# Kernel tuning notes

Hardware: AMD Instinct MI355X
Metric: run time of the kernel (lower is better)

The kernel has to match this reference:

```python
import jax, jax.numpy as jnp
import numpy as np

INPUT_DIM = 1024
OUTPUT_DIM = 1024
DEGREE = 8


def setup_inputs() -> dict:
    key = jax.random.key(0)
    k1, k2 = jax.random.split(key)
    x = jax.random.normal(k1, (8192, INPUT_DIM), dtype=jnp.float32)
    std = 1.0 / (INPUT_DIM * (DEGREE + 1))
    cheby_coeffs = jax.random.normal(k2, (INPUT_DIM, OUTPUT_DIM, DEGREE + 1), dtype=jnp.float32) * std
    return {"x": x, "cheby_coeffs": cheby_coeffs}


def reference(x, cheby_coeffs):
    # x: [B, I]; cheby_coeffs: [I, O, D+1]
    degree = cheby_coeffs.shape[-1] - 1
    t = jnp.clip(jnp.tanh(x), -0.999, 0.999)            # [B, I]
    theta = jnp.arccos(t)[..., None]                     # [B, I, 1]
    arange = jnp.arange(degree + 1, dtype=x.dtype)       # [D+1]
    basis = jnp.cos(theta * arange)                      # [B, I, D+1] Chebyshev T_d(t)
    y = jnp.einsum('bid,iod->bo', basis, cheby_coeffs)   # [B, O]
    return y
```

## Files before the change

kernel.cpp:

```cpp
#include <hip/hip_runtime.h>
#include <stdint.h>

#define B_ROWS 8192
#define I_DIM  1024
#define N_DIM  1024
#define NDEG   9
#define K_DIM  (I_DIM * (NDEG-1))

typedef __attribute__((ext_vector_type(8)))  short short8;
typedef __attribute__((ext_vector_type(16))) float f32x16;

__device__ __forceinline__ unsigned short f2bf(float f) {
  union { float f; uint32_t u; } v; v.f = f;
  uint32_t u = v.u;
  u += 0x7FFFu + ((u >> 16) & 1u);
  return (unsigned short)(u >> 16);
}

__device__ __forceinline__ float bf2f(unsigned short h) {
  union { uint32_t u; float f; } v; v.u = ((uint32_t)h) << 16;
  return v.f;
}

__device__ __forceinline__ int rowhash(int r) {
  return (r & 7) ^ ((r >> 2) & 4);
}

__global__ __launch_bounds__(256) void basis_kernel(const float* __restrict__ x,
                                                    unsigned short* __restrict__ A) {
  const int b  = blockIdx.x;
  const int i0 = threadIdx.x * 4;
  const float4 xv = *reinterpret_cast<const float4*>(x + (size_t)b * I_DIM + i0);
  float t[4];
  t[0] = fminf(fmaxf(tanhf(xv.x), -0.999f), 0.999f);
  t[1] = fminf(fmaxf(tanhf(xv.y), -0.999f), 0.999f);
  t[2] = fminf(fmaxf(tanhf(xv.z), -0.999f), 0.999f);
  t[3] = fminf(fmaxf(tanhf(xv.w), -0.999f), 0.999f);

  unsigned short* outb = A + (size_t)b * K_DIM + i0;
  float Tp[4] = {1.f, 1.f, 1.f, 1.f};
  float Tc[4] = {t[0], t[1], t[2], t[3]};
  #pragma unroll
  for (int d = 1; d < NDEG; ++d) {
    ushort4 o4;
    o4.x = f2bf(Tc[0]); o4.y = f2bf(Tc[1]); o4.z = f2bf(Tc[2]); o4.w = f2bf(Tc[3]);
    *reinterpret_cast<ushort4*>(outb + (size_t)(d - 1) * I_DIM) = o4;
    if (d < NDEG - 1) {
      #pragma unroll
      for (int j = 0; j < 4; ++j) {
        float Tn = 2.0f * t[j] * Tc[j] - Tp[j];
        Tp[j] = Tc[j]; Tc[j] = Tn;
      }
    }
  }
}

__global__ __launch_bounds__(256) void repack_kernel(const float* __restrict__ cf,
                                                     unsigned short* __restrict__ Bt,
                                                     float* __restrict__ bias) {
  __shared__ unsigned short L[32][584];
  const int i0  = blockIdx.x * 32;
  const int o0  = blockIdx.y * 64;
  const int tid = threadIdx.x;

  #pragma unroll
  for (int j = 0; j < 18; ++j) {
    const int f4  = j * 256 + tid;
    const int il  = f4 / 144;
    const int odq = f4 % 144;
    const float4 v = *reinterpret_cast<const float4*>(
        cf + ((size_t)(i0 + il) * N_DIM + o0) * NDEG + (size_t)odq * 4);
    ushort4 w;
    w.x = f2bf(v.x); w.y = f2bf(v.y); w.z = f2bf(v.z); w.w = f2bf(v.w);
    *reinterpret_cast<ushort4*>(&L[il][odq * 4]) = w;
  }
  __syncthreads();

  for (int od = tid; od < 576; od += 256) {
    const int o = od / 9, d = od % 9;
    if (d == 0) {
      float s = 0.f;
      #pragma unroll
      for (int il = 0; il < 32; ++il) s += bf2f(L[il][od]);
      atomicAdd(&bias[o0 + o], s);
    } else {
      const size_t base = (size_t)(o0 + o) * K_DIM + (size_t)(d - 1) * I_DIM + i0;
      #pragma unroll
      for (int ci = 0; ci < 4; ++ci) {
        uint32_t uu[4];
        #pragma unroll
        for (int p = 0; p < 4; ++p) {
          unsigned short lo = L[ci * 8 + p * 2 + 0][od];
          unsigned short hi = L[ci * 8 + p * 2 + 1][od];
          uu[p] = (uint32_t)lo | ((uint32_t)hi << 16);
        }
        uint4 u; u.x = uu[0]; u.y = uu[1]; u.z = uu[2]; u.w = uu[3];
        *reinterpret_cast<uint4*>(Bt + base + ci * 8) = u;
      }
    }
  }
}

__global__ __launch_bounds__(256) void gemm_kernel(const unsigned short* __restrict__ A,
                                                   const unsigned short* __restrict__ Bt,
                                                   const float* __restrict__ bias,
                                                   float* __restrict__ C) {
  __shared__ unsigned short As[128 * 64];
  __shared__ unsigned short Bs[128 * 64];
  const int tid  = threadIdx.x;
  const int lane = tid & 63;
  const int wave = tid >> 6;
  const int l31  = lane & 31;
  const int half = lane >> 5;
  const int wm   = wave >> 1;
  const int wn   = wave & 1;
  const int m0   = blockIdx.x * 128;
  const int n0   = blockIdx.y * 128;

  const int sr   = tid >> 3;
  const int slot = tid & 7;

  f32x16 acc[2][2];
  #pragma unroll
  for (int a = 0; a < 2; ++a)
    #pragma unroll
    for (int b = 0; b < 2; ++b)
      #pragma unroll
      for (int r = 0; r < 16; ++r)
        acc[a][b][r] = 0.f;

  for (int kt = 0; kt < K_DIM / 64; ++kt) {
    const int k0 = kt * 64;
    #pragma unroll
    for (int s = 0; s < 4; ++s) {
      const int r  = s * 32 + sr;
      const int gc = slot ^ rowhash(r);
      const unsigned short* srcA = A + (size_t)(m0 + r) * K_DIM + k0 + gc * 8;
      __builtin_amdgcn_global_load_lds(
          (const __attribute__((address_space(1))) void*)srcA,
          (__attribute__((address_space(3))) void*)&As[r * 64 + slot * 8], 16, 0, 0);
      const unsigned short* srcB = Bt + (size_t)(n0 + r) * K_DIM + k0 + gc * 8;
      __builtin_amdgcn_global_load_lds(
          (const __attribute__((address_space(1))) void*)srcB,
          (__attribute__((address_space(3))) void*)&Bs[r * 64 + slot * 8], 16, 0, 0);
    }
    __syncthreads();

    short8 av[2][4], bv[2][4];
    #pragma unroll
    for (int mi = 0; mi < 2; ++mi) {
      const int row = wm * 64 + mi * 32 + l31;
      #pragma unroll
      for (int ks = 0; ks < 4; ++ks) {
        const int c  = ks * 2 + half;
        const int sl = c ^ rowhash(row);
        av[mi][ks] = *reinterpret_cast<const short8*>(&As[row * 64 + sl * 8]);
      }
    }
    #pragma unroll
    for (int ni = 0; ni < 2; ++ni) {
      const int row = wn * 64 + ni * 32 + l31;
      #pragma unroll
      for (int ks = 0; ks < 4; ++ks) {
        const int c  = ks * 2 + half;
        const int sl = c ^ rowhash(row);
        bv[ni][ks] = *reinterpret_cast<const short8*>(&Bs[row * 64 + sl * 8]);
      }
    }
    #pragma unroll
    for (int ks = 0; ks < 4; ++ks)
      #pragma unroll
      for (int mi = 0; mi < 2; ++mi)
        #pragma unroll
        for (int ni = 0; ni < 2; ++ni)
          acc[mi][ni] = __builtin_amdgcn_mfma_f32_32x32x16_bf16(av[mi][ks], bv[ni][ks],
                                                                acc[mi][ni], 0, 0, 0);
    __syncthreads();
  }

  #pragma unroll
  for (int ni = 0; ni < 2; ++ni) {
    const int col  = n0 + wn * 64 + ni * 32 + l31;
    const float bc = bias[col];
    #pragma unroll
    for (int mi = 0; mi < 2; ++mi) {
      const int rbase = m0 + wm * 64 + mi * 32 + 4 * half;
      #pragma unroll
      for (int r = 0; r < 16; ++r) {
        const int row = rbase + (r & 3) + 8 * (r >> 2);
        C[(size_t)row * N_DIM + col] = acc[mi][ni][r] + bc;
      }
    }
  }
}

extern "C" void kernel_launch(void* const* d_in, const int* in_sizes, int n_in,
                              void* d_out, int out_size, void* d_ws, size_t ws_size,
                              hipStream_t stream) {
  const float* x      = (const float*)d_in[0];
  const float* coeffs = (const float*)d_in[1];
  float* y            = (float*)d_out;

  const size_t bt_bytes = (size_t)N_DIM * K_DIM * sizeof(unsigned short);
  unsigned short* Bt = (unsigned short*)d_ws;
  float* bias        = (float*)((char*)d_ws + bt_bytes);
  unsigned short* A  = (unsigned short*)((char*)d_ws + bt_bytes + 4096);

  hipMemsetAsync(bias, 0, N_DIM * sizeof(float), stream);

  repack_kernel<<<dim3(I_DIM / 32, N_DIM / 64), 256, 0, stream>>>(coeffs, Bt, bias);

  size_t avail    = (ws_size > bt_bytes + 4096) ? (ws_size - bt_bytes - 4096) : 0;
  size_t rows_fit = avail / ((size_t)K_DIM * sizeof(unsigned short));
  int m_chunk = (int)((rows_fit / 128) * 128);
  if (m_chunk > B_ROWS) m_chunk = B_ROWS;
  if (m_chunk < 128)    m_chunk = 128;

  for (int m0 = 0; m0 < B_ROWS; m0 += m_chunk) {
    int mc = B_ROWS - m0; if (mc > m_chunk) mc = m_chunk;
    basis_kernel<<<mc, 256, 0, stream>>>(x + (size_t)m0 * I_DIM, A);
    gemm_kernel<<<dim3(mc / 128, N_DIM / 128), 256, 0, stream>>>(
        A, Bt, bias, y + (size_t)m0 * N_DIM);
  }
}
```

Before: 273.9 us.

## Double-buffer A tile in LDS and load B fragments directly into registers

The GEMM now double-buffers the A tile in shared memory, prefetching the next K-slice while the current one is consumed, and keeps a single barrier per iteration. The B operand bypasses LDS: each wave loads its MFMA fragments straight from global memory into registers and prefetches the next slice. This aims to overlap global loads with MFMA work and halve LDS traffic. The cost is higher register pressure and uncoalesced 16-byte global loads for B, where the two waves sharing a column tile each fetch the same B data.

```diff
diff --git a/kernel.cpp b/kernel.cpp
--- a/kernel.cpp
+++ b/kernel.cpp
@@ -6,6 +6,7 @@
 #define N_DIM  1024
 #define NDEG   9
 #define K_DIM  (I_DIM * (NDEG-1))
+#define KT_CNT (K_DIM / 64)
 
 typedef __attribute__((ext_vector_type(8)))  short short8;
 typedef __attribute__((ext_vector_type(16))) float f32x16;
@@ -105,8 +106,7 @@
                                                    const unsigned short* __restrict__ Bt,
                                                    const float* __restrict__ bias,
                                                    float* __restrict__ C) {
-  __shared__ unsigned short As[128 * 64];
-  __shared__ unsigned short Bs[128 * 64];
+  __shared__ unsigned short As[2][128 * 64];
   const int tid  = threadIdx.x;
   const int lane = tid & 63;
   const int wave = tid >> 6;
@@ -120,6 +120,9 @@
   const int sr   = tid >> 3;
   const int slot = tid & 7;
 
+  const unsigned short* brow0 = Bt + (size_t)(n0 + wn * 64 + l31)      * K_DIM + half * 8;
+  const unsigned short* brow1 = Bt + (size_t)(n0 + wn * 64 + 32 + l31) * K_DIM + half * 8;
+
   f32x16 acc[2][2];
   #pragma unroll
   for (int a = 0; a < 2; ++a)
@@ -129,53 +132,67 @@
       for (int r = 0; r < 16; ++r)
         acc[a][b][r] = 0.f;
 
-  for (int kt = 0; kt < K_DIM / 64; ++kt) {
-    const int k0 = kt * 64;
-    #pragma unroll
-    for (int s = 0; s < 4; ++s) {
-      const int r  = s * 32 + sr;
-      const int gc = slot ^ rowhash(r);
-      const unsigned short* srcA = A + (size_t)(m0 + r) * K_DIM + k0 + gc * 8;
-      __builtin_amdgcn_global_load_lds(
-          (const __attribute__((address_space(1))) void*)srcA,
-          (__attribute__((address_space(3))) void*)&As[r * 64 + slot * 8], 16, 0, 0);
-      const unsigned short* srcB = Bt + (size_t)(n0 + r) * K_DIM + k0 + gc * 8;
-      __builtin_amdgcn_global_load_lds(
-          (const __attribute__((address_space(1))) void*)srcB,
-          (__attribute__((address_space(3))) void*)&Bs[r * 64 + slot * 8], 16, 0, 0);
-    }
+  #pragma unroll
+  for (int s = 0; s < 4; ++s) {
+    const int r  = s * 32 + sr;
+    const int gc = slot ^ rowhash(r);
+    const unsigned short* srcA = A + (size_t)(m0 + r) * K_DIM + gc * 8;
+    __builtin_amdgcn_global_load_lds(
+        (const __attribute__((address_space(1))) void*)srcA,
+        (__attribute__((address_space(3))) void*)&As[0][r * 64 + slot * 8], 16, 0, 0);
+  }
+  short8 bcur[2][4], bnxt[2][4];
+  #pragma unroll
+  for (int ks = 0; ks < 4; ++ks) {
+    bcur[0][ks] = *reinterpret_cast<const short8*>(brow0 + ks * 16);
+    bcur[1][ks] = *reinterpret_cast<const short8*>(brow1 + ks * 16);
+  }
+
+  #pragma unroll 2
+  for (int kt = 0; kt < KT_CNT; ++kt) {
+    const int p = kt & 1;
     __syncthreads();
 
-    short8 av[2][4], bv[2][4];
-    #pragma unroll
-    for (int mi = 0; mi < 2; ++mi) {
-      const int row = wm * 64 + mi * 32 + l31;
+    if (kt + 1 < KT_CNT) {
+      const int k0n = (kt + 1) * 64;
+      #pragma unroll
+      for (int s = 0; s < 4; ++s) {
+        const int r  = s * 32 + sr;
+        const int gc = slot ^ rowhash(r);
+        const unsigned short* srcA = A + (size_t)(m0 + r) * K_DIM + k0n + gc * 8;
+        __builtin_amdgcn_global_load_lds(
+            (const __attribute__((address_space(1))) void*)srcA,
+            (__attribute__((address_space(3))) void*)&As[p ^ 1][r * 64 + slot * 8], 16, 0, 0);
+      }
       #pragma unroll
       for (int ks = 0; ks < 4; ++ks) {
-        const int c  = ks * 2 + half;
-        const int sl = c ^ rowhash(row);
-        av[mi][ks] = *reinterpret_cast<const short8*>(&As[row * 64 + sl * 8]);
-      }
-    }
-    #pragma unroll
-    for (int ni = 0; ni < 2; ++ni) {
-      const int row = wn * 64 + ni * 32 + l31;
-      #pragma unroll
-      for (int ks = 0; ks < 4; ++ks) {
-        const int c  = ks * 2 + half;
-        const int sl = c ^ rowhash(row);
-        bv[ni][ks] = *reinterpret_cast<const short8*>(&Bs[row * 64 + sl * 8]);
-      }
-    }
-    #pragma unroll
-    for (int ks = 0; ks < 4; ++ks)
+        bnxt[0][ks] = *reinterpret_cast<const short8*>(brow0 + k0n + ks * 16);
+        bnxt[1][ks] = *reinterpret_cast<const short8*>(brow1 + k0n + ks * 16);
+      }
+    }
+
+    #pragma unroll
+    for (int ks = 0; ks < 4; ++ks) {
+      short8 av[2];
+      #pragma unroll
+      for (int mi = 0; mi < 2; ++mi) {
+        const int row = wm * 64 + mi * 32 + l31;
+        const int sl  = (ks * 2 + half) ^ rowhash(row);
+        av[mi] = *reinterpret_cast<const short8*>(&As[p][row * 64 + sl * 8]);
+      }
       #pragma unroll
       for (int mi = 0; mi < 2; ++mi)
         #pragma unroll
         for (int ni = 0; ni < 2; ++ni)
-          acc[mi][ni] = __builtin_amdgcn_mfma_f32_32x32x16_bf16(av[mi][ks], bv[ni][ks],
+          acc[mi][ni] = __builtin_amdgcn_mfma_f32_32x32x16_bf16(av[mi], bcur[ni][ks],
                                                                 acc[mi][ni], 0, 0, 0);
-    __syncthreads();
+    }
+
+    #pragma unroll
+    for (int ni = 0; ni < 2; ++ni)
+      #pragma unroll
+      for (int ks = 0; ks < 4; ++ks)
+        bcur[ni][ks] = bnxt[ni][ks];
   }
 
   #pragma unroll
```

Measured after the change: 408.1 us. +49.0%, slower.
